# Kernel optimization log

Hardware: AMD Instinct MI355X
Metric: run time of the kernel (lower is better)

The kernel has to match this reference:

```python
import jax, jax.numpy as jnp
import numpy as np

D_K = 64


def setup_inputs() -> dict:
    key = jax.random.key(0)
    k1, k2, k3 = jax.random.split(key, 3)
    B, H, S, DK, DV = 2, 16, 2048, 64, 64
    Q = jax.random.normal(k1, (B, H, S, DK), dtype=jnp.float32)
    K = jax.random.normal(k2, (B, H, S, DK), dtype=jnp.float32)
    V = jax.random.normal(k3, (B, H, S, DV), dtype=jnp.float32)
    # causal mask, True = keep (broadcasts over batch/head as in the torch code)
    mask = jnp.tril(jnp.ones((S, S), dtype=bool))
    return {"Q": Q, "K": K, "V": V, "mask": mask}


def reference(Q, K, V, mask):
    # scores[b,h,c,v] = sum_k Q[b,h,c,k] * K[b,h,v,k]
    scores = jnp.einsum('bhck,bhvk->bhcv', Q, K)
    # torch: B = inf at ~mask; scores - B  ->  -inf at masked positions
    scores = jnp.where(mask, scores, -jnp.inf)
    # scale applied AFTER masking, exactly as in the torch forward
    probs = jax.nn.softmax(scores / jnp.sqrt(jnp.float32(D_K)), axis=-1)
    return probs @ V
```

## Files before the change

### kernel.cpp

```cpp
#include <hip/hip_runtime.h>
#include <hip/hip_bf16.h>

#define S_LEN 2048
#define DIM   64
#define NBH   32
#define NQT   32
#define TILE_SH 12288
#define WS_NEED ((size_t)NBH * NQT * TILE_SH * sizeof(short))

typedef __attribute__((ext_vector_type(4))) float f32x4;
typedef __attribute__((ext_vector_type(8))) short s16x8;
typedef __attribute__((ext_vector_type(4))) short s16x4;

#define MFMA_B16(A,B,C) __builtin_amdgcn_mfma_f32_16x16x32_bf16(A,B,C,0,0,0)

__device__ __forceinline__ short f2bf(float x){
  union{float f;unsigned u;} v; v.f=x;
  unsigned r = v.u + 0x7FFFu + ((v.u>>16)&1u);
  return (short)(r>>16);
}
__device__ __forceinline__ float bf2f(short s){
  union{float f;unsigned u;} v; v.u=((unsigned)(unsigned short)s)<<16;
  return v.f;
}
__device__ __forceinline__ unsigned packbf(float a, float b){
  __hip_bfloat162 h = __float22bfloat162_rn(make_float2(a, b));
  union { __hip_bfloat162 h; unsigned u; } cv; cv.h = h; return cv.u;
}
__device__ __forceinline__ int swz(int row){
  return (((row&7) ^ ((row>>2)&7)) << 3);
}

__global__ __launch_bounds__(256) void prep_kv(
    const float* __restrict__ K, const float* __restrict__ V, short* __restrict__ W)
{
  const int b  = blockIdx.x;
  const int bh = b >> 5, t = b & 31;
  const float* Kt = K + ((size_t)bh * S_LEN + t * 64) * DIM;
  const float* Vt = V + ((size_t)bh * S_LEN + t * 64) * DIM;
  short* Wt = W + (size_t)b * TILE_SH;
  const int tid = threadIdx.x;
#pragma unroll
  for (int i = 0; i < 2; ++i) {
    const int m = i * 256 + tid;
    const int r = m >> 3, g = m & 7;
    const int c0 = (g << 3) ^ swz(r);
    float x[8];
    *(f32x4*)&x[0] = *(const f32x4*)(Kt + r * DIM + c0);
    *(f32x4*)&x[4] = *(const f32x4*)(Kt + r * DIM + c0 + 4);
    s16x8 hi, lo;
#pragma unroll
    for (int j = 0; j < 8; ++j) {
      short h = f2bf(x[j]);
      hi[j] = h;
      lo[j] = f2bf(x[j] - bf2f(h));
    }
    *(s16x8*)&Wt[m * 8]        = hi;
    *(s16x8*)&Wt[4096 + m * 8] = lo;
    const int dv = r;
    const int k0 = (g << 3) ^ swz(dv);
    s16x8 vv;
#pragma unroll
    for (int j = 0; j < 8; ++j) vv[j] = f2bf(Vt[(size_t)(k0 + j) * DIM + dv]);
    *(s16x8*)&Wt[8192 + m * 8] = vv;
  }
}

__device__ __forceinline__ void stage24(const short* __restrict__ src, short* dst,
                                        int w, int l) {
#pragma unroll
  for (int q = 0; q < 6; ++q) {
    const int off = (q * 4 + w) << 10;
    __builtin_amdgcn_global_load_lds(
        (const __attribute__((address_space(1))) unsigned*)((const char*)src + off + l * 16),
        (__attribute__((address_space(3))) unsigned*)((char*)dst + off),
        16, 0, 0);
  }
}

__global__ __launch_bounds__(256, 4) void fattn_main(
    const float* __restrict__ Qg, float* __restrict__ Og, const short* __restrict__ W)
{
  __shared__ __attribute__((aligned(16))) short buf[2][TILE_SH];

  const int bid0 = blockIdx.x;
  const int xcd = bid0 & 7, idx = bid0 >> 3;
  const int bh = (xcd << 2) + (idx >> 5);
  const int qt = 31 - (idx & 31);

  const int tid = threadIdx.x;
  const int w = tid >> 6, l = tid & 63;
  const int l15 = l & 15, lg = l >> 4;

  const short* Wb = W + (size_t)bh * NQT * TILE_SH;
  const float* Qb = Qg + (size_t)bh * S_LEN * DIM;
  float*       Ob = Og + (size_t)bh * S_LEN * DIM;

  const int qg = qt * 64 + w * 16 + l15;
  const float SC = 0.125f * 1.44269504088896f;

  s16x8 qh[2], ql[2];
#pragma unroll
  for (int s = 0; s < 2; ++s) {
    const float* qp = Qb + (size_t)qg * DIM + (lg << 3) + s * 32;
    float qv[8];
    *(f32x4*)&qv[0] = *(const f32x4*)qp;
    *(f32x4*)&qv[4] = *(const f32x4*)(qp + 4);
#pragma unroll
    for (int j = 0; j < 8; ++j) {
      short h = f2bf(qv[j]);
      qh[s][j] = h;
      ql[s][j] = f2bf(qv[j] - bf2f(h));
    }
  }

  f32x4 o[4];
#pragma unroll
  for (int d = 0; d < 4; ++d) o[d] = f32x4{0.f,0.f,0.f,0.f};
  float m = -INFINITY, lsum = 0.f;

  const int nt = qt + 1;
  stage24(Wb, buf[0], w, l);
  __syncthreads();
  int cur = 0;

  const int src0 = l15 + ((lg & 1) << 5);
  const int src1 = src0 + 16;
  const bool hiH = (lg >= 2);

  for (int t = 0; t < nt; ++t) {
    if (t + 1 < nt) stage24(Wb + (size_t)(t + 1) * TILE_SH, buf[cur ^ 1], w, l);

    const short* bK  = buf[cur];
    const short* bKl = bK + 4096;
    const short* bVt = bK + 8192;

    f32x4 acc[4];
#pragma unroll
    for (int f = 0; f < 4; ++f) acc[f] = f32x4{0.f,0.f,0.f,0.f};
#pragma unroll
    for (int f = 0; f < 4; ++f) {
      const int kr = f * 16 + l15;
#pragma unroll
      for (int s = 0; s < 2; ++s) {
        const int dk = (((lg << 3) + (s << 5)) ^ swz(kr));
        s16x8 ah = *(const s16x8*)&bK [kr * DIM + dk];
        s16x8 al = *(const s16x8*)&bKl[kr * DIM + dk];
        acc[f] = MFMA_B16(ah, qh[s], acc[f]);
        acc[f] = MFMA_B16(ah, ql[s], acc[f]);
        acc[f] = MFMA_B16(al, qh[s], acc[f]);
      }
    }

    const bool diag = (t == qt);
    const int kv0 = t * 64;
    float pm = -INFINITY;
#pragma unroll
    for (int f = 0; f < 4; ++f)
#pragma unroll
      for (int r = 0; r < 4; ++r) {
        float zz = acc[f][r] * SC;
        if (diag && (kv0 + f * 16 + (lg << 2) + r) > qg) zz = -INFINITY;
        acc[f][r] = zz;
        pm = fmaxf(pm, zz);
      }
    pm = fmaxf(pm, __shfl_xor(pm, 16));
    pm = fmaxf(pm, __shfl_xor(pm, 32));

    if (!__all(pm <= m)) {
      const float mn = fmaxf(m, pm);
      const float al = exp2f(m - mn);
      m = mn; lsum *= al;
#pragma unroll
      for (int d = 0; d < 4; ++d) o[d] *= al;
    }
    float rs = 0.f;
#pragma unroll
    for (int f = 0; f < 4; ++f)
#pragma unroll
      for (int r = 0; r < 4; ++r) {
        const float pv = exp2f(acc[f][r] - m);
        acc[f][r] = pv;
        rs += pv;
      }
    rs += __shfl_xor(rs, 16);
    rs += __shfl_xor(rs, 32);
    lsum += rs;

    unsigned U[4][2];
#pragma unroll
    for (int f = 0; f < 4; ++f) {
      U[f][0] = packbf(acc[f][0], acc[f][1]);
      U[f][1] = packbf(acc[f][2], acc[f][3]);
    }
#pragma unroll
    for (int s = 0; s < 2; ++s) {
      unsigned a0 = __shfl(U[2*s][0], src0), a1 = __shfl(U[2*s+1][0], src0);
      unsigned b0 = __shfl(U[2*s][1], src0), b1 = __shfl(U[2*s+1][1], src0);
      unsigned c0 = __shfl(U[2*s][0], src1), c1 = __shfl(U[2*s+1][0], src1);
      unsigned d0 = __shfl(U[2*s][1], src1), d1 = __shfl(U[2*s+1][1], src1);
      union { unsigned u[4]; s16x8 v; } pb;
      pb.u[0] = hiH ? a1 : a0;
      pb.u[1] = hiH ? b1 : b0;
      pb.u[2] = hiH ? c1 : c0;
      pb.u[3] = hiH ? d1 : d0;
      const int kv8 = (lg << 3) + (s << 5);
#pragma unroll
      for (int d = 0; d < 4; ++d) {
        const int dv = d * 16 + l15;
        s16x8 vf = *(const s16x8*)&bVt[dv * DIM + (kv8 ^ swz(dv))];
        o[d] = MFMA_B16(vf, pb.v, o[d]);
      }
    }

    __syncthreads();
    cur ^= 1;
  }

  const float inv = 1.0f / lsum;
#pragma unroll
  for (int d = 0; d < 4; ++d) {
    f32x4 ov;
#pragma unroll
    for (int r = 0; r < 4; ++r) ov[r] = o[d][r] * inv;
    *(f32x4*)(Ob + (size_t)qg * DIM + d * 16 + (lg << 2)) = ov;
  }
}

#define QBLK  64
#define KVBLK 64
#define NPAIR (NQT/2)
#define NBLK  (NBH*NPAIR)

__global__ __launch_bounds__(256) void fattn_fb(
    const float* __restrict__ Qg, const float* __restrict__ Kg,
    const float* __restrict__ Vg, float* __restrict__ Og)
{
  __shared__ __attribute__((aligned(16))) short Khi[KVBLK*DIM];
  __shared__ __attribute__((aligned(16))) short Klo[KVBLK*DIM];
  __shared__ __attribute__((aligned(16))) short Vt [DIM*KVBLK];
  __shared__ __attribute__((aligned(16))) short Pl [4*16*KVBLK];

  int bid0 = blockIdx.x;
  int bid  = (bid0 & 7) * (NBLK/8) + (bid0 >> 3);
  int bh   = bid / NPAIR;
  int pr   = bid % NPAIR;
  const int tid = threadIdx.x;
  const int w = tid >> 6, l = tid & 63, l15 = l & 15, lg = l >> 4;
  const float* Qb = Qg + (size_t)bh * S_LEN * DIM;
  const float* Kb = Kg + (size_t)bh * S_LEN * DIM;
  const float* Vb = Vg + (size_t)bh * S_LEN * DIM;
  float*       Ob = Og + (size_t)bh * S_LEN * DIM;
  const float SC = 0.125f * 1.44269504088896f;

  for (int half = 0; half < 2; ++half) {
    const int qt = half ? (NQT - 1 - pr) : pr;
    const int qg = qt * QBLK + w * 16 + l15;
    s16x8 qh[2], ql[2];
#pragma unroll
    for (int s = 0; s < 2; ++s) {
      const float* qp = Qb + (size_t)qg * DIM + (lg << 3) + s * 32;
      float qv[8];
      *(f32x4*)&qv[0] = *(const f32x4*)qp;
      *(f32x4*)&qv[4] = *(const f32x4*)(qp + 4);
#pragma unroll
      for (int j = 0; j < 8; ++j) {
        short h = f2bf(qv[j]); qh[s][j] = h; ql[s][j] = f2bf(qv[j] - bf2f(h));
      }
    }
    f32x4 o[4];
#pragma unroll
    for (int d = 0; d < 4; ++d) o[d] = f32x4{0.f,0.f,0.f,0.f};
    float m = -INFINITY, lsum = 0.f;
    const int ntiles = qt + 1;
    for (int t = 0; t < ntiles; ++t) {
      const int kv0 = t * KVBLK;
      __syncthreads();
      {
        const int row = tid >> 4, c4 = (tid & 15) << 2;
#pragma unroll
        for (int i = 0; i < 4; ++i) {
          const int r = row + (i << 4);
          const f32x4 kv4 = *(const f32x4*)(Kb + (size_t)(kv0 + r) * DIM + c4);
          const f32x4 vv4 = *(const f32x4*)(Vb + (size_t)(kv0 + r) * DIM + c4);
          const int cs = c4 ^ swz(r);
          s16x4 kh, kl;
#pragma unroll
          for (int j = 0; j < 4; ++j) { short h = f2bf(kv4[j]); kh[j] = h; kl[j] = f2bf(kv4[j] - bf2f(h)); }
          *(s16x4*)&Khi[r * DIM + cs] = kh;
          *(s16x4*)&Klo[r * DIM + cs] = kl;
#pragma unroll
          for (int j = 0; j < 4; ++j) { const int dv = c4 + j; Vt[dv * KVBLK + (r ^ swz(dv))] = f2bf(vv4[j]); }
        }
      }
      __syncthreads();
      f32x4 acc[4];
#pragma unroll
      for (int f = 0; f < 4; ++f) acc[f] = f32x4{0.f,0.f,0.f,0.f};
#pragma unroll
      for (int f = 0; f < 4; ++f) {
        const int kr = f * 16 + l15;
#pragma unroll
        for (int s = 0; s < 2; ++s) {
          const int dk = (((lg << 3) + (s << 5)) ^ swz(kr));
          s16x8 ah = *(const s16x8*)&Khi[kr * DIM + dk];
          s16x8 al = *(const s16x8*)&Klo[kr * DIM + dk];
          acc[f] = MFMA_B16(ah, qh[s], acc[f]);
          acc[f] = MFMA_B16(ah, ql[s], acc[f]);
          acc[f] = MFMA_B16(al, qh[s], acc[f]);
        }
      }
      const bool diag = (t == qt);
      float z[4][4];
#pragma unroll
      for (int f = 0; f < 4; ++f)
#pragma unroll
        for (int r = 0; r < 4; ++r) {
          float zz = acc[f][r] * SC;
          if (diag && (kv0 + f * 16 + (lg << 2) + r) > qg) zz = -INFINITY;
          z[f][r] = zz;
        }
      float pm = z[0][0];
#pragma unroll
      for (int f = 0; f < 4; ++f)
#pragma unroll
        for (int r = 0; r < 4; ++r) pm = fmaxf(pm, z[f][r]);
      pm = fmaxf(pm, __shfl_xor(pm, 16));
      pm = fmaxf(pm, __shfl_xor(pm, 32));
      const float mn = fmaxf(m, pm);
      const float alpha = exp2f(m - mn);
      float p[4][4]; float rs = 0.f;
#pragma unroll
      for (int f = 0; f < 4; ++f)
#pragma unroll
        for (int r = 0; r < 4; ++r) { const float pv = exp2f(z[f][r] - mn); p[f][r] = pv; rs += pv; }
      rs += __shfl_xor(rs, 16);
      rs += __shfl_xor(rs, 32);
      lsum = lsum * alpha + rs;
      m = mn;
#pragma unroll
      for (int d = 0; d < 4; ++d) o[d] *= alpha;
      short* Pw = &Pl[w * 16 * KVBLK];
#pragma unroll
      for (int f = 0; f < 4; ++f) {
        s16x4 pk;
#pragma unroll
        for (int r = 0; r < 4; ++r) pk[r] = f2bf(p[f][r]);
        const int kvc = (f * 16 + (lg << 2)) ^ swz(l15);
        *(s16x4*)&Pw[l15 * KVBLK + kvc] = pk;
      }
#pragma unroll
      for (int s = 0; s < 2; ++s) {
        const int kv8 = (lg << 3) + s * 32;
        s16x8 pf = *(const s16x8*)&Pw[l15 * KVBLK + (kv8 ^ swz(l15))];
#pragma unroll
        for (int d = 0; d < 4; ++d) {
          const int dv = d * 16 + l15;
          s16x8 vf = *(const s16x8*)&Vt[dv * KVBLK + (kv8 ^ swz(dv))];
          o[d] = MFMA_B16(vf, pf, o[d]);
        }
      }
    }
    const float inv = 1.0f / lsum;
#pragma unroll
    for (int d = 0; d < 4; ++d) {
      f32x4 ov;
#pragma unroll
      for (int r = 0; r < 4; ++r) ov[r] = o[d][r] * inv;
      *(f32x4*)(Ob + (size_t)qg * DIM + d * 16 + (lg << 2)) = ov;
    }
  }
}

extern "C" void kernel_launch(void* const* d_in, const int* in_sizes, int n_in,
                              void* d_out, int out_size, void* d_ws, size_t ws_size,
                              hipStream_t stream) {
  const float* Q = (const float*)d_in[0];
  const float* K = (const float*)d_in[1];
  const float* V = (const float*)d_in[2];
  float* O = (float*)d_out;
  if (ws_size >= WS_NEED) {
    short* W = (short*)d_ws;
    prep_kv  <<<dim3(NBH * NQT), dim3(256), 0, stream>>>(K, V, W);
    fattn_main<<<dim3(NBH * NQT), dim3(256), 0, stream>>>(Q, O, W);
  } else {
    fattn_fb<<<dim3(NBLK), dim3(256), 0, stream>>>(Q, K, V, O);
  }
}
```

Before: 197.1 us.

## Use 128-row query blocks with 512 threads sharing staged KV tiles

Result: faster. 167.1 us (-15.2%).

```diff
diff --git a/kernel.cpp b/kernel.cpp
--- a/kernel.cpp
+++ b/kernel.cpp
@@ -5,6 +5,7 @@
 #define DIM   64
 #define NBH   32
 #define NQT   32
+#define NQB   16
 #define TILE_SH 12288
 #define WS_NEED ((size_t)NBH * NQT * TILE_SH * sizeof(short))
 
@@ -13,6 +14,7 @@
 typedef __attribute__((ext_vector_type(4))) short s16x4;
 
 #define MFMA_B16(A,B,C) __builtin_amdgcn_mfma_f32_16x16x32_bf16(A,B,C,0,0,0)
+#define EX2(x) __builtin_amdgcn_exp2f(x)
 
 __device__ __forceinline__ short f2bf(float x){
   union{float f;unsigned u;} v; v.f=x;
@@ -34,12 +36,14 @@
 __global__ __launch_bounds__(256) void prep_kv(
     const float* __restrict__ K, const float* __restrict__ V, short* __restrict__ W)
 {
+  __shared__ short Vl[4096];
   const int b  = blockIdx.x;
   const int bh = b >> 5, t = b & 31;
   const float* Kt = K + ((size_t)bh * S_LEN + t * 64) * DIM;
   const float* Vt = V + ((size_t)bh * S_LEN + t * 64) * DIM;
   short* Wt = W + (size_t)b * TILE_SH;
   const int tid = threadIdx.x;
+
 #pragma unroll
   for (int i = 0; i < 2; ++i) {
     const int m = i * 256 + tid;
@@ -57,20 +61,34 @@
     }
     *(s16x8*)&Wt[m * 8]        = hi;
     *(s16x8*)&Wt[4096 + m * 8] = lo;
-    const int dv = r;
-    const int k0 = (g << 3) ^ swz(dv);
-    s16x8 vv;
-#pragma unroll
-    for (int j = 0; j < 8; ++j) vv[j] = f2bf(Vt[(size_t)(k0 + j) * DIM + dv]);
-    *(s16x8*)&Wt[8192 + m * 8] = vv;
+  }
+
+  {
+    const int r = tid >> 2;
+    const int cb = (tid & 3) << 4;
+    float x[16];
+#pragma unroll
+    for (int q = 0; q < 4; ++q)
+      *(f32x4*)&x[q * 4] = *(const f32x4*)(Vt + r * DIM + cb + q * 4);
+#pragma unroll
+    for (int j = 0; j < 16; ++j) {
+      const int c = cb + j;
+      Vl[c * 64 + (r ^ swz(c))] = f2bf(x[j]);
+    }
+  }
+  __syncthreads();
+#pragma unroll
+  for (int i = 0; i < 2; ++i) {
+    const int p = (i * 256 + tid) * 8;
+    *(s16x8*)&Wt[8192 + p] = *(const s16x8*)&Vl[p];
   }
 }
 
 __device__ __forceinline__ void stage24(const short* __restrict__ src, short* dst,
                                         int w, int l) {
 #pragma unroll
-  for (int q = 0; q < 6; ++q) {
-    const int off = (q * 4 + w) << 10;
+  for (int q = 0; q < 3; ++q) {
+    const int off = (q * 8 + w) << 10;
     __builtin_amdgcn_global_load_lds(
         (const __attribute__((address_space(1))) unsigned*)((const char*)src + off + l * 16),
         (__attribute__((address_space(3))) unsigned*)((char*)dst + off),
@@ -78,15 +96,14 @@
   }
 }
 
-__global__ __launch_bounds__(256, 4) void fattn_main(
+__global__ __launch_bounds__(512, 2) void fattn_main(
     const float* __restrict__ Qg, float* __restrict__ Og, const short* __restrict__ W)
 {
   __shared__ __attribute__((aligned(16))) short buf[2][TILE_SH];
 
-  const int bid0 = blockIdx.x;
-  const int xcd = bid0 & 7, idx = bid0 >> 3;
-  const int bh = (xcd << 2) + (idx >> 5);
-  const int qt = 31 - (idx & 31);
+  const int bid = blockIdx.x;
+  const int bh = bid & 31;
+  const int qt = (NQB - 1) - (bid >> 5);
 
   const int tid = threadIdx.x;
   const int w = tid >> 6, l = tid & 63;
@@ -96,7 +113,7 @@
   const float* Qb = Qg + (size_t)bh * S_LEN * DIM;
   float*       Ob = Og + (size_t)bh * S_LEN * DIM;
 
-  const int qg = qt * 64 + w * 16 + l15;
+  const int qg = qt * 128 + w * 16 + l15;
   const float SC = 0.125f * 1.44269504088896f;
 
   s16x8 qh[2], ql[2];
@@ -119,7 +136,8 @@
   for (int d = 0; d < 4; ++d) o[d] = f32x4{0.f,0.f,0.f,0.f};
   float m = -INFINITY, lsum = 0.f;
 
-  const int nt = qt + 1;
+  const int nt = 2 * qt + 2;
+  const int my_nt = nt - (w < 4 ? 1 : 0);
   stage24(Wb, buf[0], w, l);
   __syncthreads();
   int cur = 0;
@@ -131,85 +149,87 @@
   for (int t = 0; t < nt; ++t) {
     if (t + 1 < nt) stage24(Wb + (size_t)(t + 1) * TILE_SH, buf[cur ^ 1], w, l);
 
-    const short* bK  = buf[cur];
-    const short* bKl = bK + 4096;
-    const short* bVt = bK + 8192;
-
-    f32x4 acc[4];
-#pragma unroll
-    for (int f = 0; f < 4; ++f) acc[f] = f32x4{0.f,0.f,0.f,0.f};
-#pragma unroll
-    for (int f = 0; f < 4; ++f) {
-      const int kr = f * 16 + l15;
+    if (t < my_nt) {
+      const short* bK  = buf[cur];
+      const short* bKl = bK + 4096;
+      const short* bVt = bK + 8192;
+
+      f32x4 acc[4];
+#pragma unroll
+      for (int f = 0; f < 4; ++f) acc[f] = f32x4{0.f,0.f,0.f,0.f};
+#pragma unroll
+      for (int f = 0; f < 4; ++f) {
+        const int kr = f * 16 + l15;
+#pragma unroll
+        for (int s = 0; s < 2; ++s) {
+          const int dk = (((lg << 3) + (s << 5)) ^ swz(kr));
+          s16x8 ah = *(const s16x8*)&bK [kr * DIM + dk];
+          s16x8 al = *(const s16x8*)&bKl[kr * DIM + dk];
+          acc[f] = MFMA_B16(ah, qh[s], acc[f]);
+          acc[f] = MFMA_B16(ah, ql[s], acc[f]);
+          acc[f] = MFMA_B16(al, qh[s], acc[f]);
+        }
+      }
+
+      const bool diag = (t == my_nt - 1);
+      const int kv0 = t * 64;
+      float pm = -INFINITY;
+#pragma unroll
+      for (int f = 0; f < 4; ++f)
+#pragma unroll
+        for (int r = 0; r < 4; ++r) {
+          float zz = acc[f][r] * SC;
+          if (diag && (kv0 + f * 16 + (lg << 2) + r) > qg) zz = -INFINITY;
+          acc[f][r] = zz;
+          pm = fmaxf(pm, zz);
+        }
+      pm = fmaxf(pm, __shfl_xor(pm, 16));
+      pm = fmaxf(pm, __shfl_xor(pm, 32));
+
+      if (!__all(pm <= m)) {
+        const float mn = fmaxf(m, pm);
+        const float al = EX2(m - mn);
+        m = mn; lsum *= al;
+#pragma unroll
+        for (int d = 0; d < 4; ++d) o[d] *= al;
+      }
+      float rs = 0.f;
+#pragma unroll
+      for (int f = 0; f < 4; ++f)
+#pragma unroll
+        for (int r = 0; r < 4; ++r) {
+          const float pv = EX2(acc[f][r] - m);
+          acc[f][r] = pv;
+          rs += pv;
+        }
+      rs += __shfl_xor(rs, 16);
+      rs += __shfl_xor(rs, 32);
+      lsum += rs;
+
+      unsigned U[4][2];
+#pragma unroll
+      for (int f = 0; f < 4; ++f) {
+        U[f][0] = packbf(acc[f][0], acc[f][1]);
+        U[f][1] = packbf(acc[f][2], acc[f][3]);
+      }
 #pragma unroll
       for (int s = 0; s < 2; ++s) {
-        const int dk = (((lg << 3) + (s << 5)) ^ swz(kr));
-        s16x8 ah = *(const s16x8*)&bK [kr * DIM + dk];
-        s16x8 al = *(const s16x8*)&bKl[kr * DIM + dk];
-        acc[f] = MFMA_B16(ah, qh[s], acc[f]);
-        acc[f] = MFMA_B16(ah, ql[s], acc[f]);
-        acc[f] = MFMA_B16(al, qh[s], acc[f]);
-      }
-    }
-
-    const bool diag = (t == qt);
-    const int kv0 = t * 64;
-    float pm = -INFINITY;
-#pragma unroll
-    for (int f = 0; f < 4; ++f)
-#pragma unroll
-      for (int r = 0; r < 4; ++r) {
-        float zz = acc[f][r] * SC;
-        if (diag && (kv0 + f * 16 + (lg << 2) + r) > qg) zz = -INFINITY;
-        acc[f][r] = zz;
-        pm = fmaxf(pm, zz);
-      }
-    pm = fmaxf(pm, __shfl_xor(pm, 16));
-    pm = fmaxf(pm, __shfl_xor(pm, 32));
-
-    if (!__all(pm <= m)) {
-      const float mn = fmaxf(m, pm);
-      const float al = exp2f(m - mn);
-      m = mn; lsum *= al;
-#pragma unroll
-      for (int d = 0; d < 4; ++d) o[d] *= al;
-    }
-    float rs = 0.f;
-#pragma unroll
-    for (int f = 0; f < 4; ++f)
-#pragma unroll
-      for (int r = 0; r < 4; ++r) {
-        const float pv = exp2f(acc[f][r] - m);
-        acc[f][r] = pv;
-        rs += pv;
-      }
-    rs += __shfl_xor(rs, 16);
-    rs += __shfl_xor(rs, 32);
-    lsum += rs;
-
-    unsigned U[4][2];
-#pragma unroll
-    for (int f = 0; f < 4; ++f) {
-      U[f][0] = packbf(acc[f][0], acc[f][1]);
-      U[f][1] = packbf(acc[f][2], acc[f][3]);
-    }
-#pragma unroll
-    for (int s = 0; s < 2; ++s) {
-      unsigned a0 = __shfl(U[2*s][0], src0), a1 = __shfl(U[2*s+1][0], src0);
-      unsigned b0 = __shfl(U[2*s][1], src0), b1 = __shfl(U[2*s+1][1], src0);
-      unsigned c0 = __shfl(U[2*s][0], src1), c1 = __shfl(U[2*s+1][0], src1);
-      unsigned d0 = __shfl(U[2*s][1], src1), d1 = __shfl(U[2*s+1][1], src1);
-      union { unsigned u[4]; s16x8 v; } pb;
-      pb.u[0] = hiH ? a1 : a0;
-      pb.u[1] = hiH ? b1 : b0;
-      pb.u[2] = hiH ? c1 : c0;
-      pb.u[3] = hiH ? d1 : d0;
-      const int kv8 = (lg << 3) + (s << 5);
-#pragma unroll
-      for (int d = 0; d < 4; ++d) {
-        const int dv = d * 16 + l15;
-        s16x8 vf = *(const s16x8*)&bVt[dv * DIM + (kv8 ^ swz(dv))];
-        o[d] = MFMA_B16(vf, pb.v, o[d]);
+        unsigned a0 = __shfl(U[2*s][0], src0), a1 = __shfl(U[2*s+1][0], src0);
+        unsigned b0 = __shfl(U[2*s][1], src0), b1 = __shfl(U[2*s+1][1], src0);
+        unsigned c0 = __shfl(U[2*s][0], src1), c1 = __shfl(U[2*s+1][0], src1);
+        unsigned d0 = __shfl(U[2*s][1], src1), d1 = __shfl(U[2*s+1][1], src1);
+        union { unsigned u[4]; s16x8 v; } pb;
+        pb.u[0] = hiH ? a1 : a0;
+        pb.u[1] = hiH ? b1 : b0;
+        pb.u[2] = hiH ? c1 : c0;
+        pb.u[3] = hiH ? d1 : d0;
+        const int kv8 = (lg << 3) + (s << 5);
+#pragma unroll
+        for (int d = 0; d < 4; ++d) {
+          const int dv = d * 16 + l15;
+          s16x8 vf = *(const s16x8*)&bVt[dv * DIM + (kv8 ^ swz(dv))];
+          o[d] = MFMA_B16(vf, pb.v, o[d]);
+        }
       }
     }
 
@@ -328,12 +348,12 @@
       pm = fmaxf(pm, __shfl_xor(pm, 16));
       pm = fmaxf(pm, __shfl_xor(pm, 32));
       const float mn = fmaxf(m, pm);
-      const float alpha = exp2f(m - mn);
+      const float alpha = EX2(m - mn);
       float p[4][4]; float rs = 0.f;
 #pragma unroll
       for (int f = 0; f < 4; ++f)
 #pragma unroll
-        for (int r = 0; r < 4; ++r) { const float pv = exp2f(z[f][r] - mn); p[f][r] = pv; rs += pv; }
+        for (int r = 0; r < 4; ++r) { const float pv = EX2(z[f][r] - mn); p[f][r] = pv; rs += pv; }
       rs += __shfl_xor(rs, 16);
       rs += __shfl_xor(rs, 32);
       lsum = lsum * alpha + rs;
@@ -382,7 +402,7 @@
   if (ws_size >= WS_NEED) {
     short* W = (short*)d_ws;
     prep_kv  <<<dim3(NBH * NQT), dim3(256), 0, stream>>>(K, V, W);
-    fattn_main<<<dim3(NBH * NQT), dim3(256), 0, stream>>>(Q, O, W);
+    fattn_main<<<dim3(NBH * NQB), dim3(512), 0, stream>>>(Q, O, W);
   } else {
     fattn_fb<<<dim3(NBLK), dim3(256), 0, stream>>>(Q, K, V, O);
   }
```
